# Performance work log

Hardware: AMD Instinct MI355X
Metric: run time of the kernel (lower is better)

The kernel has to match this reference:

```python
import jax, jax.numpy as jnp
from jax import lax
import numpy as np

B, I, T, H = 128, 512, 256, 1024


def setup_inputs() -> dict:
    key = jax.random.key(0)
    k1, k2, k3, k4, k5 = jax.random.split(key, 5)
    s = 1.0 / np.sqrt(H)  # PyTorch LSTM init scale
    return {
        "x": jax.random.normal(k1, (B, I, T), jnp.float32),
        "W_ih": jax.random.uniform(k2, (4 * H, I), jnp.float32, -s, s),
        "W_hh": jax.random.uniform(k3, (4 * H, H), jnp.float32, -s, s),
        "b_ih": jax.random.uniform(k4, (4 * H,), jnp.float32, -s, s),
        "b_hh": jax.random.uniform(k5, (4 * H,), jnp.float32, -s, s),
    }


def reference(x, W_ih, W_hh, b_ih, b_hh):
    # x: [B, I, T] -> module transposes to [B, T, I]; scan over time.
    xs = jnp.transpose(x, (2, 0, 1))  # [T, B, I]
    # Precompute input projections for all timesteps (one big GEMM).
    x_proj = jnp.einsum('tbi,gi->tbg', xs, W_ih) + b_ih + b_hh  # [T, B, 4H]
    H_ = W_hh.shape[1]

    def step(carry, xp):
        h, c = carry
        gates = xp + h @ W_hh.T  # [B, 4H]
        i, f, g, o = jnp.split(gates, 4, axis=-1)  # PyTorch gate order i,f,g,o
        i = jax.nn.sigmoid(i)
        f = jax.nn.sigmoid(f)
        g = jnp.tanh(g)
        o = jax.nn.sigmoid(o)
        c = f * c + i * g
        h = o * jnp.tanh(c)
        return (h, c), None

    h0 = jnp.zeros((x.shape[0], H_), x.dtype)
    (h, _), _ = lax.scan(step, (h0, h0), x_proj)
    return h  # [B, H] == h_t.squeeze(0)
```

## Files before the change

### kernel.cpp

```cpp
#include <hip/hip_runtime.h>
#include <hip/hip_bf16.h>
#include <cstdint>
#include <cstddef>

#define B_ 128
#define I_ 512
#define T_ 256
#define H_ 1024

typedef __attribute__((ext_vector_type(8))) short short8;
typedef __attribute__((ext_vector_type(4))) float floatx4;
typedef __attribute__((ext_vector_type(16))) float floatx16;

static __device__ __forceinline__ unsigned short f2bf(float f) {
  unsigned u = __float_as_uint(f);
  u += 0x7FFFu + ((u >> 16) & 1u);
  return (unsigned short)(u >> 16);
}
static __device__ __forceinline__ short8 pack_bf8(floatx4 a, floatx4 b) {
  short8 v;
  v[0] = (short)f2bf(a[0]); v[1] = (short)f2bf(a[1]);
  v[2] = (short)f2bf(a[2]); v[3] = (short)f2bf(a[3]);
  v[4] = (short)f2bf(b[0]); v[5] = (short)f2bf(b[1]);
  v[6] = (short)f2bf(b[2]); v[7] = (short)f2bf(b[3]);
  return v;
}
static __device__ __forceinline__ floatx16 zero16() {
  return (floatx16){0.f,0.f,0.f,0.f,0.f,0.f,0.f,0.f,
                    0.f,0.f,0.f,0.f,0.f,0.f,0.f,0.f};
}

__global__ void __launch_bounds__(256) k_transpose(
    const float* __restrict__ x, unsigned short* __restrict__ xs) {
  __shared__ float tile[64][65];
  const int b  = blockIdx.x;
  const int i0 = blockIdx.y * 64;
  const int t0 = blockIdx.z * 64;
  const int tid = threadIdx.x;
  const int c = tid & 63, r4 = tid >> 6;
  const float* src = x + (size_t)b * I_ * T_ + (size_t)i0 * T_ + t0;
#pragma unroll
  for (int it = 0; it < 16; ++it) {
    const int r = it * 4 + r4;
    tile[r][c] = src[(size_t)r * T_ + c];
  }
  __syncthreads();
#pragma unroll
  for (int it = 0; it < 16; ++it) {
    const int tr = it * 4 + r4;
    xs[((size_t)(t0 + tr) * B_ + b) * I_ + i0 + c] = f2bf(tile[c][tr]);
  }
}

__global__ void __launch_bounds__(256, 1) k_lstm(
    const unsigned short* __restrict__ xs,
    const float* __restrict__ Whh,
    const float* __restrict__ Wih,
    const float* __restrict__ bih,
    const float* __restrict__ bhh,
    unsigned short* __restrict__ hring,
    float* __restrict__ out,
    unsigned int* __restrict__ flags)
{
  extern __shared__ char smem[];
  unsigned short (*hst)[32][264] = (unsigned short (*)[32][264])smem;
  float (*gx)[32][33] = (float (*)[32][33])(smem + 101376);

  const int wg = blockIdx.x, tid = threadIdx.x;
  const int lane = tid & 63, wave = tid >> 6;
  const int gp = wave >> 1, kh = wave & 1;
  const int bt = wg & 3, jt = wg >> 2;
  const int b0 = bt * 32, j0 = jt * 16;
  const int arow = lane & 31;
  const int hi = lane >> 5;
  const int gate = gp * 2 + (arow >> 4);
  const int wcol = j0 + (arow & 15);
  const size_t HBUF = (size_t)B_ * H_;

  short8 whf[32];
  {
    const float* wrow = Whh + (size_t)(gate * H_ + wcol) * H_ + kh * 512;
#pragma unroll
    for (int kc = 0; kc < 32; ++kc) {
      floatx4 wa = *(const floatx4*)(wrow + kc * 16 + hi * 8);
      floatx4 wb = *(const floatx4*)(wrow + kc * 16 + hi * 8 + 4);
      whf[kc] = pack_bf8(wa, wb);
    }
  }
  short8 wif[16];
  {
    const float* irow = Wih + (size_t)(gate * H_ + wcol) * I_ + kh * 256;
#pragma unroll
    for (int kc = 0; kc < 16; ++kc) {
      floatx4 wa = *(const floatx4*)(irow + kc * 16 + hi * 8);
      floatx4 wb = *(const floatx4*)(irow + kc * 16 + hi * 8 + 4);
      wif[kc] = pack_bf8(wa, wb);
    }
  }

  const int eb = tid >> 3;
  const int ejp = tid & 7;
  float bias[4][2];
#pragma unroll
  for (int q = 0; q < 4; ++q)
#pragma unroll
    for (int jj = 0; jj < 2; ++jj)
      bias[q][jj] = bih[q * H_ + j0 + ejp * 2 + jj] + bhh[q * H_ + j0 + ejp * 2 + jj];

  const int srow = tid >> 3;
  const int sq = tid & 7;

  float c0 = 0.f, c1 = 0.f;

  for (int t = 0; t < T_; ++t) {
    const unsigned short* hin = hring + (size_t)t * HBUF;
    unsigned short* hout = hring + (size_t)((t + 1) & 255) * HBUF;
    const unsigned short* xrow = xs + ((size_t)t * B_ + b0 + srow) * I_ + sq * 8;
    const unsigned short* hrow = hin + (size_t)(b0 + srow) * H_ + sq * 8;

    short8 xv[8];
#pragma unroll
    for (int c2 = 0; c2 < 2; ++c2)
#pragma unroll
      for (int p = 0; p < 4; ++p)
        xv[c2 * 4 + p] = *(const short8*)(xrow + c2 * 256 + p * 64);
#pragma unroll
    for (int c2 = 0; c2 < 2; ++c2)
#pragma unroll
      for (int p = 0; p < 4; ++p)
        *(short8*)&hst[c2][srow][sq * 8 + p * 64] = xv[c2 * 4 + p];
    __syncthreads();

    floatx16 accxa = zero16(), accxb = zero16();
    floatx16 ah0 = zero16(), ah1 = zero16();

    if (t > 0 && wave == 0) {
      const unsigned tgt = (unsigned)t;
      for (;;) {
        unsigned v = __hip_atomic_load(&flags[(bt + 4 * lane) * 16],
                                       __ATOMIC_RELAXED, __HIP_MEMORY_SCOPE_AGENT);
        if (__ballot(v >= tgt) == ~0ull) break;
        __builtin_amdgcn_s_sleep(1);
      }
    }

#pragma unroll
    for (int kc = 0; kc < 16; ++kc) {
      short8 a = *(const short8*)&hst[kh][arow][kc * 16 + hi * 8];
      if (kc & 1)
        accxb = __builtin_amdgcn_mfma_f32_32x32x16_bf16(a, wif[kc], accxb, 0, 0, 0);
      else
        accxa = __builtin_amdgcn_mfma_f32_32x32x16_bf16(a, wif[kc], accxa, 0, 0, 0);
    }
    __syncthreads();

    if (t > 0) {
      short8 hv8[16];
#pragma unroll
      for (int k = 0; k < 16; ++k)
        hv8[k] = *(const short8*)(hrow + (k >> 2) * 256 + (k & 3) * 64);

#pragma unroll
      for (int ch = 0; ch < 4; ++ch)
#pragma unroll
        for (int p = 0; p < 4; ++p)
          *(short8*)&hst[2 + ch][srow][sq * 8 + p * 64] = hv8[ch * 4 + p];
      __syncthreads();
#pragma unroll
      for (int ch2 = 0; ch2 < 2; ++ch2)
#pragma unroll
        for (int kc = 0; kc < 16; ++kc) {
          short8 a = *(const short8*)&hst[2 + 2 * kh + ch2][arow][kc * 16 + hi * 8];
          if (ch2 == 0)
            ah0 = __builtin_amdgcn_mfma_f32_32x32x16_bf16(a, whf[kc], ah0, 0, 0, 0);
          else
            ah1 = __builtin_amdgcn_mfma_f32_32x32x16_bf16(a, whf[16 + kc], ah1, 0, 0, 0);
        }
    }

#pragma unroll
    for (int r = 0; r < 16; ++r) {
      const int row = (r & 3) + 8 * (r >> 2) + 4 * hi;
      gx[wave][row][arow] = accxa[r] + accxb[r] + ah0[r] + ah1[r];
    }
    __syncthreads();

    float hv0 = 0.f, hv1 = 0.f;
#pragma unroll
    for (int jj = 0; jj < 2; ++jj) {
      const int j = ejp * 2 + jj;
      float gi = gx[0][eb][j]      + gx[1][eb][j]      + bias[0][jj];
      float gf = gx[0][eb][16 + j] + gx[1][eb][16 + j] + bias[1][jj];
      float gg = gx[2][eb][j]      + gx[3][eb][j]      + bias[2][jj];
      float go = gx[2][eb][16 + j] + gx[3][eb][16 + j] + bias[3][jj];
      float si = 1.f / (1.f + __expf(-gi));
      float sf = 1.f / (1.f + __expf(-gf));
      float tg = 2.f / (1.f + __expf(-2.f * gg)) - 1.f;
      float so = 1.f / (1.f + __expf(-go));
      float& cc = jj ? c1 : c0;
      cc = sf * cc + si * tg;
      float th = 2.f / (1.f + __expf(-2.f * cc)) - 1.f;
      float hv = so * th;
      if (jj == 0) hv0 = hv; else hv1 = hv;
    }
    const unsigned hpack = (unsigned)f2bf(hv0) | ((unsigned)f2bf(hv1) << 16);
    __hip_atomic_store((unsigned*)(hout + (size_t)(b0 + eb) * H_ + j0 + ejp * 2),
                       hpack, __ATOMIC_RELAXED, __HIP_MEMORY_SCOPE_AGENT);
    if (t == T_ - 1) {
      out[(size_t)(b0 + eb) * H_ + j0 + ejp * 2 + 0] = hv0;
      out[(size_t)(b0 + eb) * H_ + j0 + ejp * 2 + 1] = hv1;
    }

    __syncthreads();
    if (tid == 0)
      __hip_atomic_store(&flags[wg * 16], (unsigned)(t + 1), __ATOMIC_RELAXED,
                         __HIP_MEMORY_SCOPE_AGENT);
  }
}

extern "C" void kernel_launch(void* const* d_in, const int* in_sizes, int n_in,
                              void* d_out, int out_size, void* d_ws, size_t ws_size,
                              hipStream_t stream) {
  (void)in_sizes; (void)n_in; (void)out_size; (void)ws_size;
  const float* x   = (const float*)d_in[0];
  const float* Wih = (const float*)d_in[1];
  const float* Whh = (const float*)d_in[2];
  const float* bih = (const float*)d_in[3];
  const float* bhh = (const float*)d_in[4];
  float* out = (float*)d_out;

  char* ws = (char*)d_ws;
  unsigned short* xs = (unsigned short*)ws;
  unsigned int*   fl = (unsigned int*)  (ws + 33554432);
  unsigned short* hring = (unsigned short*)d_in[0];

  hipMemsetAsync(fl, 0, 16384, stream);

  k_transpose<<<dim3(B_, I_ / 64, T_ / 64), 256, 0, stream>>>(x, xs);

  const int LDS_TOTAL = 118272;
  hipFuncSetAttribute((const void*)k_lstm,
                      hipFuncAttributeMaxDynamicSharedMemorySize, LDS_TOTAL);
  k_lstm<<<dim3(256), dim3(256), LDS_TOTAL, stream>>>(
      xs, Whh, Wih, bih, bhh, hring, out, fl);
}
```

Before: 1.079 ms.

## Prefetch next-step x rows, use lighter barriers, and pack per-batch-tile flags contiguously

Loads the next timestep's x slice into registers while the current step runs, so global latency overlaps compute instead of stalling at step start. Replaces __syncthreads with explicit s_barrier variants that wait only on the counters each point needs (LDS-only, none, or full before the flag store). Flags are laid out contiguously per batch tile so the polling wave reads one coalesced 64-entry line rather than strided cache lines. The hand-written barriers risk memory-ordering bugs if a needed wait is missed, and the flag store still relies on vmcnt(0) to publish h before signalling.

```diff
diff --git a/kernel.cpp b/kernel.cpp
--- a/kernel.cpp
+++ b/kernel.cpp
@@ -11,6 +11,13 @@
 typedef __attribute__((ext_vector_type(8))) short short8;
 typedef __attribute__((ext_vector_type(4))) float floatx4;
 typedef __attribute__((ext_vector_type(16))) float floatx16;
+
+#define BAR_LGKM() do { asm volatile("s_waitcnt lgkmcnt(0)" ::: "memory"); \
+  __builtin_amdgcn_s_barrier(); asm volatile("" ::: "memory"); } while (0)
+#define BAR_NONE() do { asm volatile("" ::: "memory"); \
+  __builtin_amdgcn_s_barrier(); asm volatile("" ::: "memory"); } while (0)
+#define BAR_FULL() do { asm volatile("s_waitcnt vmcnt(0) lgkmcnt(0)" ::: "memory"); \
+  __builtin_amdgcn_s_barrier(); asm volatile("" ::: "memory"); } while (0)
 
 static __device__ __forceinline__ unsigned short f2bf(float f) {
   unsigned u = __float_as_uint(f);
@@ -76,6 +83,7 @@
   const int gate = gp * 2 + (arow >> 4);
   const int wcol = j0 + (arow & 15);
   const size_t HBUF = (size_t)B_ * H_;
+  const size_t XSTEP = (size_t)B_ * I_;
 
   short8 whf[32];
   {
@@ -110,35 +118,46 @@
   const int srow = tid >> 3;
   const int sq = tid & 7;
 
+  const unsigned short* xbase = xs + (size_t)(b0 + srow) * I_ + sq * 8;
+
+  short8 xv[8];
+#pragma unroll
+  for (int c2 = 0; c2 < 2; ++c2)
+#pragma unroll
+    for (int p = 0; p < 4; ++p)
+      xv[c2 * 4 + p] = *(const short8*)(xbase + c2 * 256 + p * 64);
+
   float c0 = 0.f, c1 = 0.f;
 
   for (int t = 0; t < T_; ++t) {
     const unsigned short* hin = hring + (size_t)t * HBUF;
     unsigned short* hout = hring + (size_t)((t + 1) & 255) * HBUF;
-    const unsigned short* xrow = xs + ((size_t)t * B_ + b0 + srow) * I_ + sq * 8;
     const unsigned short* hrow = hin + (size_t)(b0 + srow) * H_ + sq * 8;
 
-    short8 xv[8];
-#pragma unroll
-    for (int c2 = 0; c2 < 2; ++c2)
-#pragma unroll
-      for (int p = 0; p < 4; ++p)
-        xv[c2 * 4 + p] = *(const short8*)(xrow + c2 * 256 + p * 64);
 #pragma unroll
     for (int c2 = 0; c2 < 2; ++c2)
 #pragma unroll
       for (int p = 0; p < 4; ++p)
         *(short8*)&hst[c2][srow][sq * 8 + p * 64] = xv[c2 * 4 + p];
-    __syncthreads();
+    if (t + 1 < T_) {
+      const unsigned short* xp = xbase + (size_t)(t + 1) * XSTEP;
+#pragma unroll
+      for (int c2 = 0; c2 < 2; ++c2)
+#pragma unroll
+        for (int p = 0; p < 4; ++p)
+          xv[c2 * 4 + p] = *(const short8*)(xp + c2 * 256 + p * 64);
+    }
+    BAR_LGKM();
 
     floatx16 accxa = zero16(), accxb = zero16();
     floatx16 ah0 = zero16(), ah1 = zero16();
 
     if (t > 0 && wave == 0) {
       const unsigned tgt = (unsigned)t;
+      const unsigned int* fb = flags + bt * 64;
       for (;;) {
-        unsigned v = __hip_atomic_load(&flags[(bt + 4 * lane) * 16],
-                                       __ATOMIC_RELAXED, __HIP_MEMORY_SCOPE_AGENT);
+        unsigned v = __hip_atomic_load(&fb[lane], __ATOMIC_RELAXED,
+                                       __HIP_MEMORY_SCOPE_AGENT);
         if (__ballot(v >= tgt) == ~0ull) break;
         __builtin_amdgcn_s_sleep(1);
       }
@@ -152,7 +171,7 @@
       else
         accxa = __builtin_amdgcn_mfma_f32_32x32x16_bf16(a, wif[kc], accxa, 0, 0, 0);
     }
-    __syncthreads();
+    BAR_NONE();
 
     if (t > 0) {
       short8 hv8[16];
@@ -165,7 +184,7 @@
 #pragma unroll
         for (int p = 0; p < 4; ++p)
           *(short8*)&hst[2 + ch][srow][sq * 8 + p * 64] = hv8[ch * 4 + p];
-      __syncthreads();
+      BAR_LGKM();
 #pragma unroll
       for (int ch2 = 0; ch2 < 2; ++ch2)
 #pragma unroll
@@ -183,7 +202,7 @@
       const int row = (r & 3) + 8 * (r >> 2) + 4 * hi;
       gx[wave][row][arow] = accxa[r] + accxb[r] + ah0[r] + ah1[r];
     }
-    __syncthreads();
+    BAR_LGKM();
 
     float hv0 = 0.f, hv1 = 0.f;
 #pragma unroll
@@ -211,10 +230,10 @@
       out[(size_t)(b0 + eb) * H_ + j0 + ejp * 2 + 1] = hv1;
     }
 
-    __syncthreads();
+    BAR_FULL();
     if (tid == 0)
-      __hip_atomic_store(&flags[wg * 16], (unsigned)(t + 1), __ATOMIC_RELAXED,
-                         __HIP_MEMORY_SCOPE_AGENT);
+      __hip_atomic_store(&flags[bt * 64 + jt], (unsigned)(t + 1),
+                         __ATOMIC_RELAXED, __HIP_MEMORY_SCOPE_AGENT);
   }
 }
 
```

Measured after the change: 1.185 ms. 9.8% more time.

## Split K across all four waves with two gate accumulators per wave

Applied to the files above, without the earlier changes.

Reorganizes the per-workgroup work split. Each wave now covers a quarter of the K dimension for both gate pairs, using two independent accumulators, instead of each wave handling one gate pair over half of K. The goal is to shorten each wave's serial MFMA dependency chain on the critical recurrent path, and to halve how many hidden-state LDS rows each wave reads. In exchange, the gate-partial buffer in LDS doubles and the elementwise stage must reduce across four waves instead of two.

```diff
diff --git a/kernel.cpp b/kernel.cpp
--- a/kernel.cpp
+++ b/kernel.cpp
@@ -64,37 +64,38 @@
 {
   extern __shared__ char smem[];
   unsigned short (*hst)[32][264] = (unsigned short (*)[32][264])smem;
-  float (*gx)[32][33] = (float (*)[32][33])(smem + 101376);
+  float (*gx)[2][32][34] = (float (*)[2][32][34])(smem + 101376);
 
   const int wg = blockIdx.x, tid = threadIdx.x;
   const int lane = tid & 63, wave = tid >> 6;
-  const int gp = wave >> 1, kh = wave & 1;
   const int bt = wg & 3, jt = wg >> 2;
   const int b0 = bt * 32, j0 = jt * 16;
   const int arow = lane & 31;
   const int hi = lane >> 5;
-  const int gate = gp * 2 + (arow >> 4);
-  const int wcol = j0 + (arow & 15);
+  const int xch = wave >> 1;
+  const int xoff = (wave & 1) * 128;
+  const int hch = 2 + wave;
   const size_t HBUF = (size_t)B_ * H_;
 
-  short8 whf[32];
-  {
-    const float* wrow = Whh + (size_t)(gate * H_ + wcol) * H_ + kh * 512;
-#pragma unroll
-    for (int kc = 0; kc < 32; ++kc) {
+  short8 whf[2][16];
+  short8 wif[2][8];
+#pragma unroll
+  for (int g2 = 0; g2 < 2; ++g2) {
+    const int gate = g2 * 2 + (arow >> 4);
+    const int wcol = j0 + (arow & 15);
+    const float* wrow = Whh + (size_t)(gate * H_ + wcol) * H_ + wave * 256;
+#pragma unroll
+    for (int kc = 0; kc < 16; ++kc) {
       floatx4 wa = *(const floatx4*)(wrow + kc * 16 + hi * 8);
       floatx4 wb = *(const floatx4*)(wrow + kc * 16 + hi * 8 + 4);
-      whf[kc] = pack_bf8(wa, wb);
-    }
-  }
-  short8 wif[16];
-  {
-    const float* irow = Wih + (size_t)(gate * H_ + wcol) * I_ + kh * 256;
-#pragma unroll
-    for (int kc = 0; kc < 16; ++kc) {
+      whf[g2][kc] = pack_bf8(wa, wb);
+    }
+    const float* irow = Wih + (size_t)(gate * H_ + wcol) * I_ + wave * 128;
+#pragma unroll
+    for (int kc = 0; kc < 8; ++kc) {
       floatx4 wa = *(const floatx4*)(irow + kc * 16 + hi * 8);
       floatx4 wb = *(const floatx4*)(irow + kc * 16 + hi * 8 + 4);
-      wif[kc] = pack_bf8(wa, wb);
+      wif[g2][kc] = pack_bf8(wa, wb);
     }
   }
 
@@ -131,8 +132,7 @@
         *(short8*)&hst[c2][srow][sq * 8 + p * 64] = xv[c2 * 4 + p];
     __syncthreads();
 
-    floatx16 accxa = zero16(), accxb = zero16();
-    floatx16 ah0 = zero16(), ah1 = zero16();
+    floatx16 acc0 = zero16(), acc1 = zero16();
 
     if (t > 0 && wave == 0) {
       const unsigned tgt = (unsigned)t;
@@ -145,12 +145,10 @@
     }
 
 #pragma unroll
-    for (int kc = 0; kc < 16; ++kc) {
-      short8 a = *(const short8*)&hst[kh][arow][kc * 16 + hi * 8];
-      if (kc & 1)
-        accxb = __builtin_amdgcn_mfma_f32_32x32x16_bf16(a, wif[kc], accxb, 0, 0, 0);
-      else
-        accxa = __builtin_amdgcn_mfma_f32_32x32x16_bf16(a, wif[kc], accxa, 0, 0, 0);
+    for (int kc = 0; kc < 8; ++kc) {
+      short8 a = *(const short8*)&hst[xch][arow][xoff + kc * 16 + hi * 8];
+      acc0 = __builtin_amdgcn_mfma_f32_32x32x16_bf16(a, wif[0][kc], acc0, 0, 0, 0);
+      acc1 = __builtin_amdgcn_mfma_f32_32x32x16_bf16(a, wif[1][kc], acc1, 0, 0, 0);
     }
     __syncthreads();
 
@@ -167,32 +165,36 @@
           *(short8*)&hst[2 + ch][srow][sq * 8 + p * 64] = hv8[ch * 4 + p];
       __syncthreads();
 #pragma unroll
-      for (int ch2 = 0; ch2 < 2; ++ch2)
-#pragma unroll
-        for (int kc = 0; kc < 16; ++kc) {
-          short8 a = *(const short8*)&hst[2 + 2 * kh + ch2][arow][kc * 16 + hi * 8];
-          if (ch2 == 0)
-            ah0 = __builtin_amdgcn_mfma_f32_32x32x16_bf16(a, whf[kc], ah0, 0, 0, 0);
-          else
-            ah1 = __builtin_amdgcn_mfma_f32_32x32x16_bf16(a, whf[16 + kc], ah1, 0, 0, 0);
-        }
+      for (int kc = 0; kc < 16; ++kc) {
+        short8 a = *(const short8*)&hst[hch][arow][kc * 16 + hi * 8];
+        acc0 = __builtin_amdgcn_mfma_f32_32x32x16_bf16(a, whf[0][kc], acc0, 0, 0, 0);
+        acc1 = __builtin_amdgcn_mfma_f32_32x32x16_bf16(a, whf[1][kc], acc1, 0, 0, 0);
+      }
     }
 
 #pragma unroll
     for (int r = 0; r < 16; ++r) {
       const int row = (r & 3) + 8 * (r >> 2) + 4 * hi;
-      gx[wave][row][arow] = accxa[r] + accxb[r] + ah0[r] + ah1[r];
-    }
-    __syncthreads();
-
+      gx[wave][0][row][arow] = acc0[r];
+      gx[wave][1][row][arow] = acc1[r];
+    }
+    __syncthreads();
+
+    float2 s_i = {0.f, 0.f}, s_f = {0.f, 0.f}, s_g = {0.f, 0.f}, s_o = {0.f, 0.f};
+#pragma unroll
+    for (int w = 0; w < 4; ++w) {
+      s_i.x += gx[w][0][eb][ejp * 2];      s_i.y += gx[w][0][eb][ejp * 2 + 1];
+      s_f.x += gx[w][0][eb][16 + ejp * 2]; s_f.y += gx[w][0][eb][16 + ejp * 2 + 1];
+      s_g.x += gx[w][1][eb][ejp * 2];      s_g.y += gx[w][1][eb][ejp * 2 + 1];
+      s_o.x += gx[w][1][eb][16 + ejp * 2]; s_o.y += gx[w][1][eb][16 + ejp * 2 + 1];
+    }
     float hv0 = 0.f, hv1 = 0.f;
 #pragma unroll
     for (int jj = 0; jj < 2; ++jj) {
-      const int j = ejp * 2 + jj;
-      float gi = gx[0][eb][j]      + gx[1][eb][j]      + bias[0][jj];
-      float gf = gx[0][eb][16 + j] + gx[1][eb][16 + j] + bias[1][jj];
-      float gg = gx[2][eb][j]      + gx[3][eb][j]      + bias[2][jj];
-      float go = gx[2][eb][16 + j] + gx[3][eb][16 + j] + bias[3][jj];
+      float gi = (jj ? s_i.y : s_i.x) + bias[0][jj];
+      float gf = (jj ? s_f.y : s_f.x) + bias[1][jj];
+      float gg = (jj ? s_g.y : s_g.x) + bias[2][jj];
+      float go = (jj ? s_o.y : s_o.x) + bias[3][jj];
       float si = 1.f / (1.f + __expf(-gi));
       float sf = 1.f / (1.f + __expf(-gf));
       float tg = 2.f / (1.f + __expf(-2.f * gg)) - 1.f;
@@ -238,7 +240,7 @@
 
   k_transpose<<<dim3(B_, I_ / 64, T_ / 64), 256, 0, stream>>>(x, xs);
 
-  const int LDS_TOTAL = 118272;
+  const int LDS_TOTAL = 136192;
   hipFuncSetAttribute((const void*)k_lstm,
                       hipFuncAttributeMaxDynamicSharedMemorySize, LDS_TOTAL);
   k_lstm<<<dim3(256), dim3(256), LDS_TOTAL, stream>>>(
```

Measured after the change: 1.132 ms. 1.05x slower.

## Replace per-step flag barrier with sentinel-polled hidden-state loads

Applied to the files above, without the earlier changes.

Removes the per-workgroup step counters and the spin on them. Each block instead polls the hidden-state ring itself with relaxed atomic 64-bit loads until no word still holds the 0xFFFFFFFF sentinel. The ring is pre-filled with 0xFF by a 64 MB memset on every launch. This also drops two __syncthreads and the flag store/load round trip per timestep, shortening the serial critical path. In exchange it adds a large memset each call and relies on valid bf16 hidden values never matching the all-ones NaN pattern.

```diff
diff --git a/kernel.cpp b/kernel.cpp
--- a/kernel.cpp
+++ b/kernel.cpp
@@ -59,8 +59,7 @@
     const float* __restrict__ bih,
     const float* __restrict__ bhh,
     unsigned short* __restrict__ hring,
-    float* __restrict__ out,
-    unsigned int* __restrict__ flags)
+    float* __restrict__ out)
 {
   extern __shared__ char smem[];
   unsigned short (*hst)[32][264] = (unsigned short (*)[32][264])smem;
@@ -134,16 +133,6 @@
     floatx16 accxa = zero16(), accxb = zero16();
     floatx16 ah0 = zero16(), ah1 = zero16();
 
-    if (t > 0 && wave == 0) {
-      const unsigned tgt = (unsigned)t;
-      for (;;) {
-        unsigned v = __hip_atomic_load(&flags[(bt + 4 * lane) * 16],
-                                       __ATOMIC_RELAXED, __HIP_MEMORY_SCOPE_AGENT);
-        if (__ballot(v >= tgt) == ~0ull) break;
-        __builtin_amdgcn_s_sleep(1);
-      }
-    }
-
 #pragma unroll
     for (int kc = 0; kc < 16; ++kc) {
       short8 a = *(const short8*)&hst[kh][arow][kc * 16 + hi * 8];
@@ -152,19 +141,50 @@
       else
         accxa = __builtin_amdgcn_mfma_f32_32x32x16_bf16(a, wif[kc], accxa, 0, 0, 0);
     }
-    __syncthreads();
 
     if (t > 0) {
-      short8 hv8[16];
-#pragma unroll
-      for (int k = 0; k < 16; ++k)
-        hv8[k] = *(const short8*)(hrow + (k >> 2) * 256 + (k & 3) * 64);
+      unsigned long long hv[32];
+#pragma unroll
+      for (int k = 0; k < 32; ++k) {
+        const int k16 = k >> 1;
+        hv[k] = __hip_atomic_load(
+            (const unsigned long long*)(hrow + (k16 >> 2) * 256 +
+                                        (k16 & 3) * 64 + (k & 1) * 4),
+            __ATOMIC_RELAXED, __HIP_MEMORY_SCOPE_AGENT);
+      }
+      unsigned inv = 0;
+#pragma unroll
+      for (int k = 0; k < 32; ++k)
+        if ((unsigned)hv[k] == 0xFFFFFFFFu ||
+            (unsigned)(hv[k] >> 32) == 0xFFFFFFFFu)
+          inv |= 1u << k;
+      while (inv) {
+        __builtin_amdgcn_s_sleep(1);
+        unsigned next = 0;
+#pragma unroll
+        for (int k = 0; k < 32; ++k) {
+          if (inv & (1u << k)) {
+            const int k16 = k >> 1;
+            hv[k] = __hip_atomic_load(
+                (const unsigned long long*)(hrow + (k16 >> 2) * 256 +
+                                            (k16 & 3) * 64 + (k & 1) * 4),
+                __ATOMIC_RELAXED, __HIP_MEMORY_SCOPE_AGENT);
+            if ((unsigned)hv[k] == 0xFFFFFFFFu ||
+                (unsigned)(hv[k] >> 32) == 0xFFFFFFFFu)
+              next |= 1u << k;
+          }
+        }
+        inv = next;
+      }
 
 #pragma unroll
       for (int ch = 0; ch < 4; ++ch)
 #pragma unroll
-        for (int p = 0; p < 4; ++p)
-          *(short8*)&hst[2 + ch][srow][sq * 8 + p * 64] = hv8[ch * 4 + p];
+        for (int p = 0; p < 4; ++p) {
+          const int k16 = ch * 4 + p;
+          *(unsigned long long*)&hst[2 + ch][srow][sq * 8 + p * 64]     = hv[2 * k16];
+          *(unsigned long long*)&hst[2 + ch][srow][sq * 8 + p * 64 + 4] = hv[2 * k16 + 1];
+        }
       __syncthreads();
 #pragma unroll
       for (int ch2 = 0; ch2 < 2; ++ch2)
@@ -210,11 +230,6 @@
       out[(size_t)(b0 + eb) * H_ + j0 + ejp * 2 + 0] = hv0;
       out[(size_t)(b0 + eb) * H_ + j0 + ejp * 2 + 1] = hv1;
     }
-
-    __syncthreads();
-    if (tid == 0)
-      __hip_atomic_store(&flags[wg * 16], (unsigned)(t + 1), __ATOMIC_RELAXED,
-                         __HIP_MEMORY_SCOPE_AGENT);
   }
 }
 
@@ -231,16 +246,15 @@
 
   char* ws = (char*)d_ws;
   unsigned short* xs = (unsigned short*)ws;
-  unsigned int*   fl = (unsigned int*)  (ws + 33554432);
   unsigned short* hring = (unsigned short*)d_in[0];
 
-  hipMemsetAsync(fl, 0, 16384, stream);
-
   k_transpose<<<dim3(B_, I_ / 64, T_ / 64), 256, 0, stream>>>(x, xs);
+
+  hipMemsetAsync((void*)hring, 0xFF, (size_t)67108864, stream);
 
   const int LDS_TOTAL = 118272;
   hipFuncSetAttribute((const void*)k_lstm,
                       hipFuncAttributeMaxDynamicSharedMemorySize, LDS_TOTAL);
   k_lstm<<<dim3(256), dim3(256), LDS_TOTAL, stream>>>(
-      xs, Whh, Wih, bih, bhh, hring, out, fl);
-}
+      xs, Whh, Wih, bih, bhh, hring, out);
+}
```

After: 2.106 ms. 1.95x slower.
